# Kernel tuning notes

Measured on AMD Instinct MI355X. Metric: run time of the kernel, lower is better.

Reference implementation:

```python
import jax, jax.numpy as jnp
import numpy as np
import math

NHID = 256
QDIM = 256
T = 4096
B = 4

def setup_inputs() -> dict:
    key = jax.random.key(0)
    k1, k2, k3, k4 = jax.random.split(key, 4)
    # xavier_uniform with relu gain = sqrt(2)
    gain = math.sqrt(2.0)
    bound = gain * math.sqrt(6.0 / (NHID + QDIM))
    inputs = jax.random.normal(k1, (T, B, NHID), dtype=jnp.float32)
    W_q = jax.random.uniform(k2, (NHID, QDIM), minval=-bound, maxval=bound, dtype=jnp.float32)
    W_k = jax.random.uniform(k3, (NHID, QDIM), minval=-bound, maxval=bound, dtype=jnp.float32)
    W_v = jax.random.uniform(k4, (NHID, QDIM), minval=-bound, maxval=bound, dtype=jnp.float32)
    return {"inputs": inputs, "W_q": W_q, "W_k": W_k, "W_v": W_v}

def reference(inputs, W_q, W_k, W_v):
    # inputs: [T, B, H]. Original loops over time, recomputing attention of the
    # last token against the growing causal prefix. Step 0 emits x0 @ W_v, which
    # equals single-key softmax attention, so the whole thing is causal attention.
    scale = float(int(math.sqrt(QDIM)))  # faithful to int(math.sqrt(d)) in source
    q = jnp.einsum('tbh,hd->tbd', inputs, W_q)
    k = jnp.einsum('tbh,hd->tbd', inputs, W_k)
    v = jnp.einsum('tbh,hd->tbd', inputs, W_v)
    scores = jnp.einsum('ibd,jbd->bij', q, k) / scale  # [B, T, T]
    t = scores.shape[-1]
    causal = jnp.tril(jnp.ones((t, t), dtype=bool))
    scores = jnp.where(causal[None, :, :], scores, -jnp.inf)
    attn = jax.nn.softmax(scores, axis=-1)  # row i = attention_thru_time[i]
    results = jnp.einsum('bij,jbd->ibd', attn, v)  # [T, B, D]
    return results, attn
```

## Files before the change

kernel.cpp:

```cpp
#include <hip/hip_runtime.h>
#include <hip/hip_bf16.h>

#define T_DIM 4096
#define B_DIM 4

typedef unsigned short u16;
typedef __attribute__((ext_vector_type(4))) short s16x4;
typedef __attribute__((ext_vector_type(8))) short short8;
typedef __attribute__((ext_vector_type(8))) __bf16 bf16x8;
typedef __attribute__((ext_vector_type(4))) float f32x4;

static __device__ __forceinline__ u16 f2bf(float f) {
    union { float f; unsigned int u; } v; v.f = f;
    unsigned int u = v.u;
    u += 0x7FFFu + ((u >> 16) & 1u);
    return (u16)(u >> 16);
}

static __device__ __forceinline__ f32x4 mfma_k32(short8 a, short8 b, f32x4 c) {
    return __builtin_amdgcn_mfma_f32_16x16x32_bf16(
        __builtin_bit_cast(bf16x8, a), __builtin_bit_cast(bf16x8, b), c, 0, 0, 0);
}
static __device__ __forceinline__ f32x4 mfma_k16(s16x4 a, s16x4 b, f32x4 c) {
    return __builtin_amdgcn_mfma_f32_16x16x16bf16_1k(a, b, c, 0, 0, 0);
}

__global__ __launch_bounds__(256) void wtrans_kernel(
    const float* __restrict__ Wq, const float* __restrict__ Wk,
    const float* __restrict__ Wv, u16* __restrict__ wT) {
    int idx = blockIdx.x * 256 + threadIdx.x;
    int w   = idx >> 16;
    int rem = idx & 65535;
    int k   = rem >> 8;
    int n   = rem & 255;
    const float* W = (w == 0) ? Wq : (w == 1) ? Wk : Wv;
    wT[w * 65536 + n * 256 + k] = f2bf(W[k * 256 + n]);
}

__global__ __launch_bounds__(256, 4) void proj_kernel(
    const float* __restrict__ X, const u16* __restrict__ wT,
    u16* __restrict__ qf, u16* __restrict__ kf, u16* __restrict__ vfw) {
    const int r0  = blockIdx.x * 16;
    const int wid = threadIdx.x >> 6, lane = threadIdx.x & 63;
    const int lr  = lane & 15, lg = lane >> 4;

    short8 af[8];
    const float* xrow = X + (size_t)(r0 + lr) * 256 + lg * 8;
#pragma unroll
    for (int kc = 0; kc < 8; ++kc) {
        f32x4 xa = *(const f32x4*)(xrow + kc * 32);
        f32x4 xb = *(const f32x4*)(xrow + kc * 32 + 4);
        union { u16 u[8]; short8 v; } t;
#pragma unroll
        for (int e = 0; e < 4; ++e) { t.u[e] = f2bf(xa[e]); t.u[4 + e] = f2bf(xb[e]); }
        af[kc] = t.v;
    }

    for (int w = 0; w < 3; ++w) {
        f32x4 acc[4];
#pragma unroll
        for (int nf = 0; nf < 4; ++nf) acc[nf] = (f32x4){0.f,0.f,0.f,0.f};
        const u16* wbase = wT + w * 65536 + (size_t)(16 * (4 * wid) + lr) * 256 + lg * 8;
#pragma unroll
        for (int kc = 0; kc < 8; ++kc)
#pragma unroll
            for (int nf = 0; nf < 4; ++nf) {
                short8 bfv = *(const short8*)(wbase + nf * 16 * 256 + kc * 32);
                acc[nf] = mfma_k32(af[kc], bfv, acc[nf]);
            }
#pragma unroll
        for (int nf = 0; nf < 4; ++nf)
#pragma unroll
            for (int r = 0; r < 4; ++r) {
                int rg = r0 + 4 * lg + r;
                int t  = rg >> 2, bb = rg & 3;
                int d  = 16 * (4 * wid + nf) + lr;
                u16 val = f2bf(acc[nf][r]);
                if (w < 2) {
                    int tile = t >> 4, lrq = t & 15;
                    int kc = d >> 5, lgq = (d >> 3) & 3, e = d & 7;
                    size_t idx = ((((size_t)bb * 256 + tile) * 8 + kc) * 64
                                  + lrq + 16 * lgq) * 8 + e;
                    if (w == 0) qf[idx] = val; else kf[idx] = val;
                } else {
                    int jt = t >> 6, hh = (t >> 4) & 3;
                    int lgv = (t >> 2) & 3, el = t & 3;
                    int nfv = d >> 4, lrv = d & 15;
                    int lanev = lrv + 16 * lgv;
                    size_t idx = (((((size_t)bb * 64 + jt) * 4 + hh) * 8 + (nfv >> 1)) * 64
                                  + lanev) * 8 + (nfv & 1) * 4 + el;
                    vfw[idx] = val;
                }
            }
    }
}

__global__ __launch_bounds__(512) void attn_kernel(
    const u16* __restrict__ qf, const u16* __restrict__ kf,
    const u16* __restrict__ vfw, float* __restrict__ out) {
    __shared__ float l_sm[32];
    __shared__ float O_sm[32 * 264];

    const int blk = blockIdx.x;
    const int xcd = blk & 7;
    const int b = xcd >> 1, par = xcd & 1;
    const int pair = 2 * (blk >> 3) + par;

    const int tid = threadIdx.x;
    const int wid = tid >> 6, lane = tid & 63;
    const int f = wid >> 2, h = wid & 3;
    const int lr = lane & 15, lg = lane >> 4;

    float* attnO = out + (size_t)T_DIM * B_DIM * 256 + (size_t)b * T_DIM * T_DIM;

    for (int phase = 0; phase < 2; ++phase) {
        const int it = phase ? (127 - pair) : pair;
        const int i0 = it * 32;
        const int irow = i0 + 16 * f + lr;
        const int numJT = it / 2 + 1;

        __syncthreads();
        if (tid < 32) l_sm[tid] = 0.f;
        __syncthreads();

        short8 q8[8];
        const short8* qp = (const short8*)(qf + (((size_t)b * 256 + it * 2 + f) * 8) * 512);
#pragma unroll
        for (int kc = 0; kc < 8; ++kc) q8[kc] = qp[kc * 64 + lane];

        float rs = 0.f;
        {
            int jt = 0;
            for (; jt + 3 < numJT; jt += 4) {
                const short8* kp0 = (const short8*)(kf + (((size_t)b * 256 + jt * 4 + h) * 8) * 512);
                const short8* kp1 = kp0 + 2048;
                const short8* kp2 = kp0 + 4096;
                const short8* kp3 = kp0 + 6144;
                f32x4 a0 = {0.f,0.f,0.f,0.f}, a1 = a0, a2 = a0, a3 = a0;
#pragma unroll
                for (int kc = 0; kc < 8; ++kc) {
                    a0 = mfma_k32(kp0[kc * 64 + lane], q8[kc], a0);
                    a1 = mfma_k32(kp1[kc * 64 + lane], q8[kc], a1);
                    a2 = mfma_k32(kp2[kc * 64 + lane], q8[kc], a2);
                    a3 = mfma_k32(kp3[kc * 64 + lane], q8[kc], a3);
                }
                const int j00 = jt * 64 + 16 * h + 4 * lg;
#pragma unroll
                for (int r = 0; r < 4; ++r) {
                    rs += (j00 + r       <= irow) ? __expf(a0[r] * 0.0625f) : 0.f;
                    rs += (j00 + 64 + r  <= irow) ? __expf(a1[r] * 0.0625f) : 0.f;
                    rs += (j00 + 128 + r <= irow) ? __expf(a2[r] * 0.0625f) : 0.f;
                    rs += (j00 + 192 + r <= irow) ? __expf(a3[r] * 0.0625f) : 0.f;
                }
            }
            for (; jt + 1 < numJT; jt += 2) {
                const short8* kp0 = (const short8*)(kf + (((size_t)b * 256 + jt * 4 + h) * 8) * 512);
                const short8* kp1 = kp0 + 2048;
                f32x4 a0 = {0.f,0.f,0.f,0.f}, a1 = a0;
#pragma unroll
                for (int kc = 0; kc < 8; ++kc) {
                    a0 = mfma_k32(kp0[kc * 64 + lane], q8[kc], a0);
                    a1 = mfma_k32(kp1[kc * 64 + lane], q8[kc], a1);
                }
                const int j00 = jt * 64 + 16 * h + 4 * lg;
#pragma unroll
                for (int r = 0; r < 4; ++r) {
                    rs += (j00 + r      <= irow) ? __expf(a0[r] * 0.0625f) : 0.f;
                    rs += (j00 + 64 + r <= irow) ? __expf(a1[r] * 0.0625f) : 0.f;
                }
            }
            if (jt < numJT) {
                const short8* kp = (const short8*)(kf + (((size_t)b * 256 + jt * 4 + h) * 8) * 512);
                f32x4 a = {0.f,0.f,0.f,0.f};
#pragma unroll
                for (int kc = 0; kc < 8; ++kc)
                    a = mfma_k32(kp[kc * 64 + lane], q8[kc], a);
                const int j0 = jt * 64 + 16 * h + 4 * lg;
#pragma unroll
                for (int r = 0; r < 4; ++r)
                    rs += (j0 + r <= irow) ? __expf(a[r] * 0.0625f) : 0.f;
            }
        }
        rs += __shfl_xor(rs, 16, 64);
        rs += __shfl_xor(rs, 32, 64);
        if (lane < 16) atomicAdd(&l_sm[16 * f + lr], rs);
        __syncthreads();
        const float inv = 1.0f / l_sm[16 * f + lr];

        f32x4 oacc[16];
#pragma unroll
        for (int nf = 0; nf < 16; ++nf) oacc[nf] = (f32x4){0.f,0.f,0.f,0.f};

        {
            int jt = 0;
            for (; jt + 1 < numJT; jt += 2) {
                const short8* kp0 = (const short8*)(kf + (((size_t)b * 256 + jt * 4 + h) * 8) * 512);
                const short8* kp1 = kp0 + 2048;
                const u16* vb0 = vfw + ((((size_t)b * 64 + jt) * 4 + h) * 4096)
                               + (size_t)lane * 8;
                const u16* vb1 = vb0 + 16384;

                short8 vpre0[4], vpre1[4];
#pragma unroll
                for (int nf2 = 0; nf2 < 4; ++nf2) {
                    vpre0[nf2] = *(const short8*)(vb0 + (size_t)nf2 * 512);
                    vpre1[nf2] = *(const short8*)(vb1 + (size_t)nf2 * 512);
                }

                short8 k0[8], k1[8];
#pragma unroll
                for (int kc = 0; kc < 8; ++kc) { k0[kc] = kp0[kc * 64 + lane]; k1[kc] = kp1[kc * 64 + lane]; }
                f32x4 a0 = {0.f,0.f,0.f,0.f}, a1 = a0;
#pragma unroll
                for (int kc = 0; kc < 8; ++kc) {
                    a0 = mfma_k32(k0[kc], q8[kc], a0);
                    a1 = mfma_k32(k1[kc], q8[kc], a1);
                }
                const int j00 = jt * 64 + 16 * h + 4 * lg;
#pragma unroll
                for (int r = 0; r < 4; ++r) {
                    a0[r] = (j00 + r      <= irow) ? __expf(a0[r] * 0.0625f) * inv : 0.f;
                    a1[r] = (j00 + 64 + r <= irow) ? __expf(a1[r] * 0.0625f) * inv : 0.f;
                }
                __builtin_nontemporal_store(a0, (f32x4*)(attnO + (size_t)irow * T_DIM + j00));
                __builtin_nontemporal_store(a1, (f32x4*)(attnO + (size_t)irow * T_DIM + j00 + 64));

                union { u16 u[4]; s16x4 v; } t0, t1;
#pragma unroll
                for (int r = 0; r < 4; ++r) { t0.u[r] = f2bf(a0[r]); t1.u[r] = f2bf(a1[r]); }
                const s16x4 pk0 = t0.v, pk1 = t1.v;

#pragma unroll
                for (int nf2 = 0; nf2 < 4; ++nf2) {
                    short8 v0 = vpre0[nf2];
                    short8 v1 = vpre1[nf2];
                    oacc[2*nf2]   = mfma_k16(pk0, __builtin_shufflevector(v0, v0, 0,1,2,3), oacc[2*nf2]);
                    oacc[2*nf2+1] = mfma_k16(pk0, __builtin_shufflevector(v0, v0, 4,5,6,7), oacc[2*nf2+1]);
                    oacc[2*nf2]   = mfma_k16(pk1, __builtin_shufflevector(v1, v1, 0,1,2,3), oacc[2*nf2]);
                    oacc[2*nf2+1] = mfma_k16(pk1, __builtin_shufflevector(v1, v1, 4,5,6,7), oacc[2*nf2+1]);
                }
#pragma unroll
                for (int nf2 = 4; nf2 < 8; ++nf2) {
                    short8 v0 = *(const short8*)(vb0 + (size_t)nf2 * 512);
                    short8 v1 = *(const short8*)(vb1 + (size_t)nf2 * 512);
                    oacc[2*nf2]   = mfma_k16(pk0, __builtin_shufflevector(v0, v0, 0,1,2,3), oacc[2*nf2]);
                    oacc[2*nf2+1] = mfma_k16(pk0, __builtin_shufflevector(v0, v0, 4,5,6,7), oacc[2*nf2+1]);
                    oacc[2*nf2]   = mfma_k16(pk1, __builtin_shufflevector(v1, v1, 0,1,2,3), oacc[2*nf2]);
                    oacc[2*nf2+1] = mfma_k16(pk1, __builtin_shufflevector(v1, v1, 4,5,6,7), oacc[2*nf2+1]);
                }
            }
            if (jt < numJT) {
                const short8* kp = (const short8*)(kf + (((size_t)b * 256 + jt * 4 + h) * 8) * 512);
                f32x4 a = {0.f,0.f,0.f,0.f};
#pragma unroll
                for (int kc = 0; kc < 8; ++kc)
                    a = mfma_k32(kp[kc * 64 + lane], q8[kc], a);
                const int j0 = jt * 64 + 16 * h + 4 * lg;
#pragma unroll
                for (int r = 0; r < 4; ++r)
                    a[r] = (j0 + r <= irow) ? __expf(a[r] * 0.0625f) * inv : 0.f;
                __builtin_nontemporal_store(a, (f32x4*)(attnO + (size_t)irow * T_DIM + j0));
                union { u16 u[4]; s16x4 v; } t;
#pragma unroll
                for (int r = 0; r < 4; ++r) t.u[r] = f2bf(a[r]);
                const s16x4 pk = t.v;
                const u16* vb = vfw + ((((size_t)b * 64 + jt) * 4 + h) * 4096)
                              + (size_t)lane * 8;
#pragma unroll
                for (int nf2 = 0; nf2 < 8; ++nf2) {
                    short8 v0 = *(const short8*)(vb + (size_t)nf2 * 512);
                    oacc[2*nf2]   = mfma_k16(pk, __builtin_shufflevector(v0, v0, 0,1,2,3), oacc[2*nf2]);
                    oacc[2*nf2+1] = mfma_k16(pk, __builtin_shufflevector(v0, v0, 4,5,6,7), oacc[2*nf2+1]);
                }
            }
        }

        for (int step = 0; step < 4; ++step) {
            if (h == step) {
#pragma unroll
                for (int nf = 0; nf < 16; ++nf)
#pragma unroll
                    for (int r = 0; r < 4; ++r) {
                        int row = 16 * f + 4 * lg + r, d = 16 * nf + lr;
                        if (step == 0) O_sm[row * 264 + d] = oacc[nf][r];
                        else           O_sm[row * 264 + d] += oacc[nf][r];
                    }
            }
            __syncthreads();
        }
#pragma unroll
        for (int u = 0; u < 4; ++u) {
            int ix = tid + 512 * u;
            int row = ix >> 6, c = ix & 63;
            f32x4 v = *(const f32x4*)(O_sm + row * 264 + c * 4);
            __builtin_nontemporal_store(v,
                (f32x4*)(out + ((size_t)(i0 + row) * B_DIM + b) * 256 + c * 4));
        }
        __syncthreads();

        const int z0 = numJT * 64;
        if (z0 < T_DIM) {
            const int n4 = (T_DIM - z0) >> 2;
            for (int rr = 0; rr < 32; ++rr) {
                f32x4* rowp = (f32x4*)(attnO + (size_t)(i0 + rr) * T_DIM + z0);
                for (int c = tid; c < n4; c += 512) {
                    f32x4 z = {0.f, 0.f, 0.f, 0.f};
                    __builtin_nontemporal_store(z, rowp + c);
                }
            }
        }
    }
}

extern "C" void kernel_launch(void* const* d_in, const int* in_sizes, int n_in,
                              void* d_out, int out_size, void* d_ws, size_t ws_size,
                              hipStream_t stream) {
    (void)in_sizes; (void)n_in; (void)out_size; (void)ws_size;
    const float* X  = (const float*)d_in[0];
    const float* Wq = (const float*)d_in[1];
    const float* Wk = (const float*)d_in[2];
    const float* Wv = (const float*)d_in[3];
    float* out = (float*)d_out;

    char* ws = (char*)d_ws;
    u16* qf  = (u16*)(ws);
    u16* kf  = (u16*)(ws + (size_t)8  * 1024 * 1024);
    u16* vfw = (u16*)(ws + (size_t)16 * 1024 * 1024);
    u16* wT  = (u16*)(ws + (size_t)24 * 1024 * 1024);

    wtrans_kernel<<<dim3(768), dim3(256), 0, stream>>>(Wq, Wk, Wv, wT);
    proj_kernel<<<dim3(1024), dim3(256), 0, stream>>>(X, wT, qf, kf, vfw);
    attn_kernel<<<dim3(256), dim3(512), 0, stream>>>(qf, kf, vfw, out);
}
```

Before: 206.8 us.

## Replace two-pass softmax with single pass plus separate attention rescale kernel

Removes the first QK^T pass that only computed row sums. The attention kernel now writes unnormalized exp scores, accumulates the row sum alongside, and scales the PV accumulator by the inverse at the end. A new kernel re-reads and rescales the causal part of the attention matrix using stored inverses. This saves a QK^T recompute but adds a read-modify-write of about half of a 256 MB fp32 attention output, which is likely memory-bound and costly. It also drops max subtraction, so exp overflow is still a risk, as before.

After: 259.1 us. 25.3% more time.

```diff
diff --git a/kernel.cpp b/kernel.cpp
--- a/kernel.cpp
+++ b/kernel.cpp
@@ -97,7 +97,8 @@
 
 __global__ __launch_bounds__(512) void attn_kernel(
     const u16* __restrict__ qf, const u16* __restrict__ kf,
-    const u16* __restrict__ vfw, float* __restrict__ out) {
+    const u16* __restrict__ vfw, float* __restrict__ inv_ws,
+    float* __restrict__ out) {
     __shared__ float l_sm[32];
     __shared__ float O_sm[32 * 264];
 
@@ -129,64 +130,6 @@
         for (int kc = 0; kc < 8; ++kc) q8[kc] = qp[kc * 64 + lane];
 
         float rs = 0.f;
-        {
-            int jt = 0;
-            for (; jt + 3 < numJT; jt += 4) {
-                const short8* kp0 = (const short8*)(kf + (((size_t)b * 256 + jt * 4 + h) * 8) * 512);
-                const short8* kp1 = kp0 + 2048;
-                const short8* kp2 = kp0 + 4096;
-                const short8* kp3 = kp0 + 6144;
-                f32x4 a0 = {0.f,0.f,0.f,0.f}, a1 = a0, a2 = a0, a3 = a0;
-#pragma unroll
-                for (int kc = 0; kc < 8; ++kc) {
-                    a0 = mfma_k32(kp0[kc * 64 + lane], q8[kc], a0);
-                    a1 = mfma_k32(kp1[kc * 64 + lane], q8[kc], a1);
-                    a2 = mfma_k32(kp2[kc * 64 + lane], q8[kc], a2);
-                    a3 = mfma_k32(kp3[kc * 64 + lane], q8[kc], a3);
-                }
-                const int j00 = jt * 64 + 16 * h + 4 * lg;
-#pragma unroll
-                for (int r = 0; r < 4; ++r) {
-                    rs += (j00 + r       <= irow) ? __expf(a0[r] * 0.0625f) : 0.f;
-                    rs += (j00 + 64 + r  <= irow) ? __expf(a1[r] * 0.0625f) : 0.f;
-                    rs += (j00 + 128 + r <= irow) ? __expf(a2[r] * 0.0625f) : 0.f;
-                    rs += (j00 + 192 + r <= irow) ? __expf(a3[r] * 0.0625f) : 0.f;
-                }
-            }
-            for (; jt + 1 < numJT; jt += 2) {
-                const short8* kp0 = (const short8*)(kf + (((size_t)b * 256 + jt * 4 + h) * 8) * 512);
-                const short8* kp1 = kp0 + 2048;
-                f32x4 a0 = {0.f,0.f,0.f,0.f}, a1 = a0;
-#pragma unroll
-                for (int kc = 0; kc < 8; ++kc) {
-                    a0 = mfma_k32(kp0[kc * 64 + lane], q8[kc], a0);
-                    a1 = mfma_k32(kp1[kc * 64 + lane], q8[kc], a1);
-                }
-                const int j00 = jt * 64 + 16 * h + 4 * lg;
-#pragma unroll
-                for (int r = 0; r < 4; ++r) {
-                    rs += (j00 + r      <= irow) ? __expf(a0[r] * 0.0625f) : 0.f;
-                    rs += (j00 + 64 + r <= irow) ? __expf(a1[r] * 0.0625f) : 0.f;
-                }
-            }
-            if (jt < numJT) {
-                const short8* kp = (const short8*)(kf + (((size_t)b * 256 + jt * 4 + h) * 8) * 512);
-                f32x4 a = {0.f,0.f,0.f,0.f};
-#pragma unroll
-                for (int kc = 0; kc < 8; ++kc)
-                    a = mfma_k32(kp[kc * 64 + lane], q8[kc], a);
-                const int j0 = jt * 64 + 16 * h + 4 * lg;
-#pragma unroll
-                for (int r = 0; r < 4; ++r)
-                    rs += (j0 + r <= irow) ? __expf(a[r] * 0.0625f) : 0.f;
-            }
-        }
-        rs += __shfl_xor(rs, 16, 64);
-        rs += __shfl_xor(rs, 32, 64);
-        if (lane < 16) atomicAdd(&l_sm[16 * f + lr], rs);
-        __syncthreads();
-        const float inv = 1.0f / l_sm[16 * f + lr];
-
         f32x4 oacc[16];
 #pragma unroll
         for (int nf = 0; nf < 16; ++nf) oacc[nf] = (f32x4){0.f,0.f,0.f,0.f};
@@ -219,8 +162,9 @@
                 const int j00 = jt * 64 + 16 * h + 4 * lg;
 #pragma unroll
                 for (int r = 0; r < 4; ++r) {
-                    a0[r] = (j00 + r      <= irow) ? __expf(a0[r] * 0.0625f) * inv : 0.f;
-                    a1[r] = (j00 + 64 + r <= irow) ? __expf(a1[r] * 0.0625f) * inv : 0.f;
+                    a0[r] = (j00 + r      <= irow) ? __expf(a0[r] * 0.0625f) : 0.f;
+                    a1[r] = (j00 + 64 + r <= irow) ? __expf(a1[r] * 0.0625f) : 0.f;
+                    rs += a0[r] + a1[r];
                 }
                 __builtin_nontemporal_store(a0, (f32x4*)(attnO + (size_t)irow * T_DIM + j00));
                 __builtin_nontemporal_store(a1, (f32x4*)(attnO + (size_t)irow * T_DIM + j00 + 64));
@@ -257,8 +201,10 @@
                     a = mfma_k32(kp[kc * 64 + lane], q8[kc], a);
                 const int j0 = jt * 64 + 16 * h + 4 * lg;
 #pragma unroll
-                for (int r = 0; r < 4; ++r)
-                    a[r] = (j0 + r <= irow) ? __expf(a[r] * 0.0625f) * inv : 0.f;
+                for (int r = 0; r < 4; ++r) {
+                    a[r] = (j0 + r <= irow) ? __expf(a[r] * 0.0625f) : 0.f;
+                    rs += a[r];
+                }
                 __builtin_nontemporal_store(a, (f32x4*)(attnO + (size_t)irow * T_DIM + j0));
                 union { u16 u[4]; s16x4 v; } t;
 #pragma unroll
@@ -274,6 +220,24 @@
                 }
             }
         }
+
+        rs += __shfl_xor(rs, 16, 64);
+        rs += __shfl_xor(rs, 32, 64);
+        if (lane < 16) atomicAdd(&l_sm[16 * f + lr], rs);
+        __syncthreads();
+        if (tid < 32) {
+            float iv = 1.0f / l_sm[tid];
+            l_sm[tid] = iv;
+            inv_ws[b * T_DIM + i0 + tid] = iv;
+        }
+        __syncthreads();
+        float linv[4];
+#pragma unroll
+        for (int r = 0; r < 4; ++r) linv[r] = l_sm[16 * f + 4 * lg + r];
+#pragma unroll
+        for (int nf = 0; nf < 16; ++nf)
+#pragma unroll
+            for (int r = 0; r < 4; ++r) oacc[nf][r] *= linv[r];
 
         for (int step = 0; step < 4; ++step) {
             if (h == step) {
@@ -307,6 +271,33 @@
                     f32x4 z = {0.f, 0.f, 0.f, 0.f};
                     __builtin_nontemporal_store(z, rowp + c);
                 }
+            }
+        }
+    }
+}
+
+__global__ __launch_bounds__(512) void rescale_kernel(
+    const float* __restrict__ inv_ws, float* __restrict__ out) {
+    const int blk = blockIdx.x;
+    const int xcd = blk & 7;
+    const int b = xcd >> 1, par = xcd & 1;
+    const int pair = 2 * (blk >> 3) + par;
+
+    float* attnO = out + (size_t)T_DIM * B_DIM * 256 + (size_t)b * T_DIM * T_DIM;
+
+    for (int phase = 0; phase < 2; ++phase) {
+        const int it = phase ? (127 - pair) : pair;
+        const int i0 = it * 32;
+        const int n4 = ((it / 2 + 1) * 64) >> 2;
+        for (int rr = 0; rr < 32; ++rr) {
+            const int row = i0 + rr;
+            const float iv = inv_ws[b * T_DIM + row];
+            f32x4* rowp = (f32x4*)(attnO + (size_t)row * T_DIM);
+            for (int c = threadIdx.x; c < n4; c += 512) {
+                f32x4 v = rowp[c];
+#pragma unroll
+                for (int e = 0; e < 4; ++e) v[e] *= iv;
+                __builtin_nontemporal_store(v, rowp + c);
             }
         }
     }
@@ -327,8 +318,10 @@
     u16* kf  = (u16*)(ws + (size_t)8  * 1024 * 1024);
     u16* vfw = (u16*)(ws + (size_t)16 * 1024 * 1024);
     u16* wT  = (u16*)(ws + (size_t)24 * 1024 * 1024);
+    float* inv_ws = (float*)(ws + (size_t)25 * 1024 * 1024);
 
     wtrans_kernel<<<dim3(768), dim3(256), 0, stream>>>(Wq, Wk, Wv, wT);
     proj_kernel<<<dim3(1024), dim3(256), 0, stream>>>(X, wT, qf, kf, vfw);
-    attn_kernel<<<dim3(256), dim3(512), 0, stream>>>(qf, kf, vfw, out);
-}
+    attn_kernel<<<dim3(256), dim3(512), 0, stream>>>(qf, kf, vfw, inv_ws, out);
+    rescale_kernel<<<dim3(256), dim3(512), 0, stream>>>(inv_ws, out);
+}
```

## Split softmax row-sum pass into separate finer-grained kernel

Applied to the files above, without the earlier changes.

Moves the first pass (QK^T plus exp row sums for softmax normalisation) out of the attention kernel into its own kernel. The new kernel runs 1024 blocks over 16-row tiles and writes reciprocal row sums to workspace. The attention kernel then reads those values instead of computing them. This spreads the normalisation work across more blocks for better occupancy and load balance, at the cost of an extra launch and a global round trip for the sums.

Measured after the change: 241.8 us. +16.9%, slower.

```diff
diff --git a/kernel.cpp b/kernel.cpp
--- a/kernel.cpp
+++ b/kernel.cpp
@@ -95,10 +95,97 @@
     }
 }
 
+__global__ __launch_bounds__(256) void lsum_kernel(
+    const u16* __restrict__ qf, const u16* __restrict__ kf,
+    float* __restrict__ inv_ws) {
+    __shared__ float l_sm[16];
+
+    const int blk = blockIdx.x;
+    const int xcd = blk & 7;
+    const int b = xcd >> 1, par = xcd & 1;
+    const int idx = blk >> 3;
+    const int it16 = 2 * (127 - idx) + par;
+    const int i0 = it16 * 16;
+
+    const int wid = threadIdx.x >> 6, lane = threadIdx.x & 63;
+    const int h = wid;
+    const int lr = lane & 15, lg = lane >> 4;
+    const int irow = i0 + lr;
+    const int numJT = it16 / 4 + 1;
+
+    if (threadIdx.x < 16) l_sm[threadIdx.x] = 0.f;
+    __syncthreads();
+
+    short8 q8[8];
+    const short8* qp = (const short8*)(qf + (((size_t)b * 256 + it16) * 8) * 512);
+#pragma unroll
+    for (int kc = 0; kc < 8; ++kc) q8[kc] = qp[kc * 64 + lane];
+
+    float rs = 0.f;
+    {
+        int jt = 0;
+        for (; jt + 3 < numJT; jt += 4) {
+            const short8* kp0 = (const short8*)(kf + (((size_t)b * 256 + jt * 4 + h) * 8) * 512);
+            const short8* kp1 = kp0 + 2048;
+            const short8* kp2 = kp0 + 4096;
+            const short8* kp3 = kp0 + 6144;
+            f32x4 a0 = {0.f,0.f,0.f,0.f}, a1 = a0, a2 = a0, a3 = a0;
+#pragma unroll
+            for (int kc = 0; kc < 8; ++kc) {
+                a0 = mfma_k32(kp0[kc * 64 + lane], q8[kc], a0);
+                a1 = mfma_k32(kp1[kc * 64 + lane], q8[kc], a1);
+                a2 = mfma_k32(kp2[kc * 64 + lane], q8[kc], a2);
+                a3 = mfma_k32(kp3[kc * 64 + lane], q8[kc], a3);
+            }
+            const int j00 = jt * 64 + 16 * h + 4 * lg;
+#pragma unroll
+            for (int r = 0; r < 4; ++r) {
+                rs += (j00 + r       <= irow) ? __expf(a0[r] * 0.0625f) : 0.f;
+                rs += (j00 + 64 + r  <= irow) ? __expf(a1[r] * 0.0625f) : 0.f;
+                rs += (j00 + 128 + r <= irow) ? __expf(a2[r] * 0.0625f) : 0.f;
+                rs += (j00 + 192 + r <= irow) ? __expf(a3[r] * 0.0625f) : 0.f;
+            }
+        }
+        for (; jt + 1 < numJT; jt += 2) {
+            const short8* kp0 = (const short8*)(kf + (((size_t)b * 256 + jt * 4 + h) * 8) * 512);
+            const short8* kp1 = kp0 + 2048;
+            f32x4 a0 = {0.f,0.f,0.f,0.f}, a1 = a0;
+#pragma unroll
+            for (int kc = 0; kc < 8; ++kc) {
+                a0 = mfma_k32(kp0[kc * 64 + lane], q8[kc], a0);
+                a1 = mfma_k32(kp1[kc * 64 + lane], q8[kc], a1);
+            }
+            const int j00 = jt * 64 + 16 * h + 4 * lg;
+#pragma unroll
+            for (int r = 0; r < 4; ++r) {
+                rs += (j00 + r      <= irow) ? __expf(a0[r] * 0.0625f) : 0.f;
+                rs += (j00 + 64 + r <= irow) ? __expf(a1[r] * 0.0625f) : 0.f;
+            }
+        }
+        if (jt < numJT) {
+            const short8* kp = (const short8*)(kf + (((size_t)b * 256 + jt * 4 + h) * 8) * 512);
+            f32x4 a = {0.f,0.f,0.f,0.f};
+#pragma unroll
+            for (int kc = 0; kc < 8; ++kc)
+                a = mfma_k32(kp[kc * 64 + lane], q8[kc], a);
+            const int j0 = jt * 64 + 16 * h + 4 * lg;
+#pragma unroll
+            for (int r = 0; r < 4; ++r)
+                rs += (j0 + r <= irow) ? __expf(a[r] * 0.0625f) : 0.f;
+        }
+    }
+    rs += __shfl_xor(rs, 16, 64);
+    rs += __shfl_xor(rs, 32, 64);
+    if (lane < 16) atomicAdd(&l_sm[lr], rs);
+    __syncthreads();
+    if (threadIdx.x < 16)
+        inv_ws[b * T_DIM + i0 + threadIdx.x] = 1.0f / l_sm[threadIdx.x];
+}
+
 __global__ __launch_bounds__(512) void attn_kernel(
     const u16* __restrict__ qf, const u16* __restrict__ kf,
-    const u16* __restrict__ vfw, float* __restrict__ out) {
-    __shared__ float l_sm[32];
+    const u16* __restrict__ vfw, const float* __restrict__ inv_ws,
+    float* __restrict__ out) {
     __shared__ float O_sm[32 * 264];
 
     const int blk = blockIdx.x;
@@ -120,72 +207,13 @@
         const int numJT = it / 2 + 1;
 
         __syncthreads();
-        if (tid < 32) l_sm[tid] = 0.f;
-        __syncthreads();
 
         short8 q8[8];
         const short8* qp = (const short8*)(qf + (((size_t)b * 256 + it * 2 + f) * 8) * 512);
 #pragma unroll
         for (int kc = 0; kc < 8; ++kc) q8[kc] = qp[kc * 64 + lane];
 
-        float rs = 0.f;
-        {
-            int jt = 0;
-            for (; jt + 3 < numJT; jt += 4) {
-                const short8* kp0 = (const short8*)(kf + (((size_t)b * 256 + jt * 4 + h) * 8) * 512);
-                const short8* kp1 = kp0 + 2048;
-                const short8* kp2 = kp0 + 4096;
-                const short8* kp3 = kp0 + 6144;
-                f32x4 a0 = {0.f,0.f,0.f,0.f}, a1 = a0, a2 = a0, a3 = a0;
-#pragma unroll
-                for (int kc = 0; kc < 8; ++kc) {
-                    a0 = mfma_k32(kp0[kc * 64 + lane], q8[kc], a0);
-                    a1 = mfma_k32(kp1[kc * 64 + lane], q8[kc], a1);
-                    a2 = mfma_k32(kp2[kc * 64 + lane], q8[kc], a2);
-                    a3 = mfma_k32(kp3[kc * 64 + lane], q8[kc], a3);
-                }
-                const int j00 = jt * 64 + 16 * h + 4 * lg;
-#pragma unroll
-                for (int r = 0; r < 4; ++r) {
-                    rs += (j00 + r       <= irow) ? __expf(a0[r] * 0.0625f) : 0.f;
-                    rs += (j00 + 64 + r  <= irow) ? __expf(a1[r] * 0.0625f) : 0.f;
-                    rs += (j00 + 128 + r <= irow) ? __expf(a2[r] * 0.0625f) : 0.f;
-                    rs += (j00 + 192 + r <= irow) ? __expf(a3[r] * 0.0625f) : 0.f;
-                }
-            }
-            for (; jt + 1 < numJT; jt += 2) {
-                const short8* kp0 = (const short8*)(kf + (((size_t)b * 256 + jt * 4 + h) * 8) * 512);
-                const short8* kp1 = kp0 + 2048;
-                f32x4 a0 = {0.f,0.f,0.f,0.f}, a1 = a0;
-#pragma unroll
-                for (int kc = 0; kc < 8; ++kc) {
-                    a0 = mfma_k32(kp0[kc * 64 + lane], q8[kc], a0);
-                    a1 = mfma_k32(kp1[kc * 64 + lane], q8[kc], a1);
-                }
-                const int j00 = jt * 64 + 16 * h + 4 * lg;
-#pragma unroll
-                for (int r = 0; r < 4; ++r) {
-                    rs += (j00 + r      <= irow) ? __expf(a0[r] * 0.0625f) : 0.f;
-                    rs += (j00 + 64 + r <= irow) ? __expf(a1[r] * 0.0625f) : 0.f;
-                }
-            }
-            if (jt < numJT) {
-                const short8* kp = (const short8*)(kf + (((size_t)b * 256 + jt * 4 + h) * 8) * 512);
-                f32x4 a = {0.f,0.f,0.f,0.f};
-#pragma unroll
-                for (int kc = 0; kc < 8; ++kc)
-                    a = mfma_k32(kp[kc * 64 + lane], q8[kc], a);
-                const int j0 = jt * 64 + 16 * h + 4 * lg;
-#pragma unroll
-                for (int r = 0; r < 4; ++r)
-                    rs += (j0 + r <= irow) ? __expf(a[r] * 0.0625f) : 0.f;
-            }
-        }
-        rs += __shfl_xor(rs, 16, 64);
-        rs += __shfl_xor(rs, 32, 64);
-        if (lane < 16) atomicAdd(&l_sm[16 * f + lr], rs);
-        __syncthreads();
-        const float inv = 1.0f / l_sm[16 * f + lr];
+        const float inv = inv_ws[b * T_DIM + irow];
 
         f32x4 oacc[16];
 #pragma unroll
@@ -327,8 +355,10 @@
     u16* kf  = (u16*)(ws + (size_t)8  * 1024 * 1024);
     u16* vfw = (u16*)(ws + (size_t)16 * 1024 * 1024);
     u16* wT  = (u16*)(ws + (size_t)24 * 1024 * 1024);
+    float* inv_ws = (float*)(ws + (size_t)25 * 1024 * 1024);
 
     wtrans_kernel<<<dim3(768), dim3(256), 0, stream>>>(Wq, Wk, Wv, wT);
     proj_kernel<<<dim3(1024), dim3(256), 0, stream>>>(X, wT, qf, kf, vfw);
-    attn_kernel<<<dim3(256), dim3(512), 0, stream>>>(qf, kf, vfw, out);
-}
+    lsum_kernel<<<dim3(1024), dim3(256), 0, stream>>>(qf, kf, inv_ws);
+    attn_kernel<<<dim3(256), dim3(512), 0, stream>>>(qf, kf, vfw, inv_ws, out);
+}
```
